# Optimization experiments

Hardware: AMD Instinct MI355X
Metric: run time of the kernel (lower is better)

The kernel has to match this reference:

```python
import jax, jax.numpy as jnp
import numpy as np

B, T, D, H, O = 4096, 512, 18, 8, 1


def setup_inputs() -> dict:
    key = jax.random.key(0)
    ks = jax.random.split(key, 8)
    x = jax.random.normal(ks[0], (B, T, D), dtype=jnp.float32)
    # PackedSequence invariant: lengths sorted descending, each >= 1
    lengths = jax.random.randint(ks[1], (B,), 1, T + 1, dtype=jnp.int32)
    lengths = jnp.sort(lengths)[::-1]
    s = 1.0 / np.sqrt(H)
    W_ih = jax.random.uniform(ks[2], (4 * H, D), jnp.float32, -s, s)
    W_hh = jax.random.uniform(ks[3], (4 * H, H), jnp.float32, -s, s)
    b_ih = jax.random.uniform(ks[4], (4 * H,), jnp.float32, -s, s)
    b_hh = jax.random.uniform(ks[5], (4 * H,), jnp.float32, -s, s)
    W_lin = jax.random.uniform(ks[6], (O, H), jnp.float32, -s, s)
    b_lin = jax.random.uniform(ks[7], (O,), jnp.float32, -s, s)
    return {"x": x, "lengths": lengths, "W_ih": W_ih, "W_hh": W_hh,
            "b_ih": b_ih, "b_hh": b_hh, "W_lin": W_lin, "b_lin": b_lin}


def reference(x, lengths, W_ih, W_hh, b_ih, b_hh, W_lin, b_lin):
    # Single-layer LSTM over ragged (packed) sequences, zero init hidden,
    # then a Linear head on every valid timestep (squash_packed).
    bias = b_ih + b_hh  # [4H]
    xg = jnp.einsum('btd,gd->btg', x, W_ih) + bias  # precompute input gates [B,T,4H]
    xg_t = jnp.swapaxes(xg, 0, 1)  # [T,B,4H]
    # mask[t,b] = t < lengths[b]  (packed steps actually computed)
    mask = (jnp.arange(T)[:, None] < lengths[None, :])[..., None]  # [T,B,1]

    h0 = jnp.zeros((B, H), x.dtype)
    c0 = jnp.zeros((B, H), x.dtype)

    def step(carry, inp):
        h, c = carry
        g_x, m = inp  # [B,4H], [B,1]
        gates = g_x + h @ W_hh.T
        i, f, g, o = jnp.split(gates, 4, axis=-1)  # torch gate order i,f,g,o
        i = jax.nn.sigmoid(i); f = jax.nn.sigmoid(f); o = jax.nn.sigmoid(o)
        g = jnp.tanh(g)
        c_new = f * c + i * g
        h_new = o * jnp.tanh(c_new)
        # beyond a sequence's length the packed LSTM never updates its state
        h = jnp.where(m, h_new, h)
        c = jnp.where(m, c_new, c)
        return (h, c), jnp.where(m, h_new, 0.0)

    (_, _), hs = jax.lax.scan(step, (h0, c0), (xg_t, mask))  # hs: [T,B,H]
    hs = jnp.swapaxes(hs, 0, 1)  # [B,T,H]
    y = jnp.einsum('bth,oh->bto', hs, W_lin) + b_lin  # [B,T,O]
    # linear head only applied to valid (packed) entries; zero out padding
    pad_mask = jnp.swapaxes(mask, 0, 1)  # [B,T,1]
    return jnp.where(pad_mask, y, 0.0)
```

## Files before the change

### kernel.cpp

```cpp
#include <hip/hip_runtime.h>


namespace {

constexpr int NT = 512;
constexpr int ND = 18;
constexpr float LOG2E = 1.4426950408889634f;

typedef float v2f __attribute__((ext_vector_type(2)));
typedef float v4f __attribute__((ext_vector_type(4)));

template <int C>
__device__ __forceinline__ float fdpp(float v) {
    const int i = __float_as_int(v);
    return __int_as_float(__builtin_amdgcn_update_dpp(i, i, C, 0xF, 0xF, true));
}
__device__ __forceinline__ void gload_lds(const void* g, void* l) {
    __builtin_amdgcn_global_load_lds(
        (const __attribute__((address_space(1))) void*)g,
        (__attribute__((address_space(3))) void*)l, 4, 0, 0);
}

__global__ __launch_bounds__(128, 1) void lstm_pc(
    const float* __restrict__ x, const int* __restrict__ lengths,
    const float* __restrict__ W_ih, const float* __restrict__ W_hh,
    const float* __restrict__ b_ih, const float* __restrict__ b_hh,
    const float* __restrict__ W_lin, const float* __restrict__ b_lin,
    float* __restrict__ out)
{
    __shared__ __align__(16) float Aring[32][4][16];
    __shared__ __align__(16) float Bring[4][8][4][2];
    __shared__ __align__(16) v2f   XG[4][8][16][5];

    const int tid  = (int)threadIdx.x;
    const int wav  = tid >> 6;
    const int w    = tid & 63;
    const int grp  = w >> 4;
    const int l16  = w & 15;
    const int p    = l16 >> 3;
    const int j    = l16 & 7;
    const int lenmax = lengths[blockIdx.x * 4];
    const int nwin = (lenmax + 15) >> 4;
    const int rowA = j + (p ? 8 : 0);
    const int rowB = j + (p ? 24 : 16);

    if (wav == 1) {
        v2f wxA[9], wxB[9];
        {
            const v2f* ra = (const v2f*)(W_ih + rowA * ND);
            const v2f* rb = (const v2f*)(W_ih + rowB * ND);
#pragma unroll
            for (int k = 0; k < 9; ++k) { wxA[k] = ra[k]; wxB[k] = rb[k]; }
        }
        const float biasA = b_ih[rowA] + b_hh[rowA];
        const float biasB = b_ih[rowB] + b_hh[rowB];

        const char* xc = (const char*)x;
        const char* pA = xc + (size_t)((((unsigned)(blockIdx.x * 4 + (w >> 4)) * (NT * ND))
                                       + (unsigned)(w & 15)) * 4u);
        const char* pB = xc + (size_t)((((unsigned)(blockIdx.x * 4 + ((w >> 1) & 3)) * (NT * ND))
                                       + 16u + (unsigned)(w & 1)) * 4u);
        const unsigned rB0 = (unsigned)(w >> 3);

        auto dma_chunk = [&](int dd) {
            const int r0 = dd * 8;
#pragma unroll
            for (int k = 0; k < 8; ++k) {
                const int rr = (r0 + k < NT) ? (r0 + k) : (NT - 1);
                gload_lds(pA + (unsigned)rr * 72u, &Aring[(r0 + k) & 31][0][0]);
            }
            unsigned rb = (unsigned)r0 + rB0;
            rb = (rb < (unsigned)NT) ? rb : (unsigned)(NT - 1);
            gload_lds(pB + rb * 72u, &Bring[dd & 3][0][0][0]);
        };

        auto produce_chunk = [&](int cc) {
            const int s0 = (cc * 8) & 31;
            const int bf = cc & 3;
#pragma unroll
            for (int k = 0; k < 8; ++k) {
                const v4f* ap = (const v4f*)&Aring[s0 + k][grp][0];
                const v4f q0 = ap[0], q1 = ap[1], q2 = ap[2], q3 = ap[3];
                const v2f bt = *(const v2f*)&Bring[bf][k][grp][0];
                v2f aA = v2f{biasA, 0.f}, aB = v2f{biasB, 0.f};
                aA = q0.lo * wxA[0] + aA;  aB = q0.lo * wxB[0] + aB;
                aA = q0.hi * wxA[1] + aA;  aB = q0.hi * wxB[1] + aB;
                aA = q1.lo * wxA[2] + aA;  aB = q1.lo * wxB[2] + aB;
                aA = q1.hi * wxA[3] + aA;  aB = q1.hi * wxB[3] + aB;
                aA = q2.lo * wxA[4] + aA;  aB = q2.lo * wxB[4] + aB;
                aA = q2.hi * wxA[5] + aA;  aB = q2.hi * wxB[5] + aB;
                aA = q3.lo * wxA[6] + aA;  aB = q3.lo * wxB[6] + aB;
                aA = q3.hi * wxA[7] + aA;  aB = q3.hi * wxB[7] + aB;
                aA = bt * wxA[8] + aA;     aB = bt * wxB[8] + aB;
                XG[bf][k][l16][grp] = v2f{aA.x + aA.y, aB.x + aB.y};
            }
        };

        dma_chunk(0); dma_chunk(1); dma_chunk(2); dma_chunk(3);
        asm volatile("s_waitcnt vmcnt(18)" ::: "memory");
        produce_chunk(0);
        produce_chunk(1);
        asm volatile("s_waitcnt lgkmcnt(0)" ::: "memory");
        __builtin_amdgcn_sched_barrier(0);
        __builtin_amdgcn_s_barrier();
        __builtin_amdgcn_sched_barrier(0);

        for (int I = 0; I < nwin; ++I) {
            dma_chunk(2 * I + 4);
            dma_chunk(2 * I + 5);
            asm volatile("s_waitcnt vmcnt(18)" ::: "memory");
            produce_chunk(2 * I + 2);
            produce_chunk(2 * I + 3);
            asm volatile("s_waitcnt lgkmcnt(0)" ::: "memory");
            __builtin_amdgcn_sched_barrier(0);
            __builtin_amdgcn_s_barrier();
            __builtin_amdgcn_sched_barrier(0);
        }
    } else {
        const int len = lengths[blockIdx.x * 4 + grp];

        int idx[8];
        idx[0] = j;
        idx[1] = __builtin_amdgcn_update_dpp(0, j, 0x121, 0xF, 0xF, true) & 7;
        idx[2] = __builtin_amdgcn_update_dpp(0, j, 0x122, 0xF, 0xF, true) & 7;
        idx[3] = __builtin_amdgcn_update_dpp(0, j, 0x123, 0xF, 0xF, true) & 7;
        idx[4] = __builtin_amdgcn_update_dpp(0, j, 0x124, 0xF, 0xF, true) & 7;
        idx[5] = __builtin_amdgcn_update_dpp(0, j, 0x125, 0xF, 0xF, true) & 7;
        idx[6] = __builtin_amdgcn_update_dpp(0, j, 0x126, 0xF, 0xF, true) & 7;
        idx[7] = __builtin_amdgcn_update_dpp(0, j, 0x127, 0xF, 0xF, true) & 7;

        v2f whA[4], whB[4], wl2[4];
#pragma unroll
        for (int r = 0; r < 4; ++r) {
            whA[r] = v2f{W_hh[rowA * 8 + idx[2 * r]], W_hh[rowA * 8 + idx[2 * r + 1]]};
            whB[r] = v2f{W_hh[rowB * 8 + idx[2 * r]], W_hh[rowB * 8 + idx[2 * r + 1]]};
            wl2[r] = v2f{W_lin[idx[2 * r]], W_lin[idx[2 * r + 1]]};
        }
        const float bl = b_lin[0];
        const float Kp = p ? -LOG2E : -2.0f * LOG2E;

        float* yb = out + (size_t)(blockIdx.x * 4 + grp) * NT;

        v2f hp[4] = {v2f{0.f, 0.f}, v2f{0.f, 0.f}, v2f{0.f, 0.f}, v2f{0.f, 0.f}};
        float c_ = 0.0f, hown = 0.0f;

        __builtin_amdgcn_s_barrier();
        __builtin_amdgcn_sched_barrier(0);

        for (int I = 0; I < nwin; ++I) {
            const int t = I * 16;
            const v2f* xg0 = &XG[(2 * I) & 3][0][l16][grp];
            const v2f* xg1 = &XG[(2 * I + 1) & 3][0][l16][grp];
            float y[16];
            v2f xgn = xg0[0];
#pragma unroll
            for (int k = 0; k < 16; ++k) {
                const v2f xgc = xgn;
                if (k < 15) xgn = (k + 1 < 8) ? xg0[(k + 1) * 80] : xg1[(k + 1 - 8) * 80];

                v2f tA = hp[0] * whA[0];
                tA = hp[1] * whA[1] + tA;
                tA = hp[2] * whA[2] + tA;
                tA = hp[3] * whA[3] + tA;
                v2f tB = hp[0] * whB[0];
                tB = hp[1] * whB[1] + tB;
                tB = hp[2] * whB[2] + tB;
                tB = hp[3] * whB[3] + tB;
                const float aA = (xgc.x + tA.x) + tA.y;
                const float aB = (xgc.y + tB.x) + tB.y;

                const float vA = __builtin_amdgcn_rcpf(
                    1.0f + __builtin_amdgcn_exp2f(aA * -LOG2E));
                const float sB = __builtin_amdgcn_rcpf(
                    1.0f + __builtin_amdgcn_exp2f(aB * Kp));
                const float vB = p ? sB : fmaf(2.0f, sB, -1.0f);

                const float send1 = p ? vA : (vA * vB);
                const float ex1 = fdpp<0x128>(send1);
                const float f_ = p ? send1 : ex1;
                const float ig_ = p ? ex1 : send1;
                c_ = fmaf(f_, c_, ig_);
                const float tc = fmaf(-2.0f, __builtin_amdgcn_rcpf(
                    1.0f + __builtin_amdgcn_exp2f(c_ * (2.0f * LOG2E))), 1.0f);
                const float ex2 = fdpp<0x128>(vB);
                const float o_ = p ? vB : ex2;
                hown = o_ * tc;

                const float h1 = fdpp<0x121>(hown);
                const float h2 = fdpp<0x122>(hown);
                const float h3 = fdpp<0x123>(hown);
                const float h4 = fdpp<0x124>(hown);
                const float h5 = fdpp<0x125>(hown);
                const float h6 = fdpp<0x126>(hown);
                const float h7 = fdpp<0x127>(hown);
                hp[0] = v2f{hown, h1}; hp[1] = v2f{h2, h3};
                hp[2] = v2f{h4, h5};   hp[3] = v2f{h6, h7};

                v2f ya = hp[0] * wl2[0];
                ya = hp[1] * wl2[1] + ya;
                ya = hp[2] * wl2[2] + ya;
                ya = hp[3] * wl2[3] + ya;
                y[k] = (ya.x + ya.y) + bl;
            }

            if (l16 == 0) {
                if (t + 15 < len) {
                    *(v4f*)(yb + t)      = v4f{y[0],  y[1],  y[2],  y[3]};
                    *(v4f*)(yb + t + 4)  = v4f{y[4],  y[5],  y[6],  y[7]};
                    *(v4f*)(yb + t + 8)  = v4f{y[8],  y[9],  y[10], y[11]};
                    *(v4f*)(yb + t + 12) = v4f{y[12], y[13], y[14], y[15]};
                } else {
#pragma unroll
                    for (int k = 0; k < 16; ++k)
                        if (t + k < len) yb[t + k] = y[k];
                }
            }
            __builtin_amdgcn_sched_barrier(0);
            __builtin_amdgcn_s_barrier();
            __builtin_amdgcn_sched_barrier(0);
        }
    }
}

}

extern "C" void kernel_launch(void* const* d_in, const int* in_sizes, int n_in,
                              void* d_out, int out_size, void* d_ws, size_t ws_size,
                              hipStream_t stream) {
    const float* x     = (const float*)d_in[0];
    const int*   lens  = (const int*)d_in[1];
    const float* W_ih  = (const float*)d_in[2];
    const float* W_hh  = (const float*)d_in[3];
    const float* b_ih  = (const float*)d_in[4];
    const float* b_hh  = (const float*)d_in[5];
    const float* W_lin = (const float*)d_in[6];
    const float* b_lin = (const float*)d_in[7];
    float* out = (float*)d_out;

    hipMemsetAsync(out, 0, (size_t)4096 * NT * sizeof(float), stream);

    lstm_pc<<<1024, 128, 0, stream>>>(x, lens, W_ih, W_hh, b_ih, b_hh,
                                      W_lin, b_lin, out);
}
```

Before: 78.87 us.

## Process eight sequences per block with one lane per hidden unit

Changes the work mapping so each block handles 8 sequences instead of 4, and each lane owns one hidden unit and computes all four gates itself. Before, a pair of lanes split the gates and exchanged them with DPP. The hidden state is broadcast with shuffles, and blocks are paired long/short through a reversed index to balance the sorted lengths. This halves the grid to 512 blocks and removes cross-lane gate exchanges. In return each lane does twice the recurrent FMAs and four transcendentals per step on the serial critical path, and shuffles replace the cheaper DPP row moves.

```diff
diff --git a/kernel.cpp b/kernel.cpp
--- a/kernel.cpp
+++ b/kernel.cpp
@@ -10,56 +10,53 @@
 typedef float v2f __attribute__((ext_vector_type(2)));
 typedef float v4f __attribute__((ext_vector_type(4)));
 
-template <int C>
-__device__ __forceinline__ float fdpp(float v) {
-    const int i = __float_as_int(v);
-    return __int_as_float(__builtin_amdgcn_update_dpp(i, i, C, 0xF, 0xF, true));
-}
 __device__ __forceinline__ void gload_lds(const void* g, void* l) {
     __builtin_amdgcn_global_load_lds(
         (const __attribute__((address_space(1))) void*)g,
         (__attribute__((address_space(3))) void*)l, 4, 0, 0);
 }
 
-__global__ __launch_bounds__(128, 1) void lstm_pc(
+__global__ __launch_bounds__(128, 1) void lstm_pc8(
     const float* __restrict__ x, const int* __restrict__ lengths,
     const float* __restrict__ W_ih, const float* __restrict__ W_hh,
     const float* __restrict__ b_ih, const float* __restrict__ b_hh,
     const float* __restrict__ W_lin, const float* __restrict__ b_lin,
     float* __restrict__ out)
 {
-    __shared__ __align__(16) float Aring[32][4][16];
-    __shared__ __align__(16) float Bring[4][8][4][2];
-    __shared__ __align__(16) v2f   XG[4][8][16][5];
-
-    const int tid  = (int)threadIdx.x;
-    const int wav  = tid >> 6;
-    const int w    = tid & 63;
-    const int grp  = w >> 4;
-    const int l16  = w & 15;
-    const int p    = l16 >> 3;
-    const int j    = l16 & 7;
-    const int lenmax = lengths[blockIdx.x * 4];
+    __shared__ __align__(16) float Aring[32][8][16];
+    __shared__ __align__(16) float Bring[4][2][8][4][2];
+    __shared__ __align__(16) v4f   XG[4][8][8][8];
+
+    const int q_ = (int)blockIdx.x & 255;
+    const int g  = ((int)blockIdx.x >> 8) ? (511 - q_) : q_;
+
+    const int tid = (int)threadIdx.x;
+    const int wav = tid >> 6;
+    const int w   = tid & 63;
+    const int s   = w >> 3;
+    const int j   = w & 7;
+    const int lenmax = lengths[g * 8];
     const int nwin = (lenmax + 15) >> 4;
-    const int rowA = j + (p ? 8 : 0);
-    const int rowB = j + (p ? 24 : 16);
 
     if (wav == 1) {
-        v2f wxA[9], wxB[9];
-        {
-            const v2f* ra = (const v2f*)(W_ih + rowA * ND);
-            const v2f* rb = (const v2f*)(W_ih + rowB * ND);
-#pragma unroll
-            for (int k = 0; k < 9; ++k) { wxA[k] = ra[k]; wxB[k] = rb[k]; }
-        }
-        const float biasA = b_ih[rowA] + b_hh[rowA];
-        const float biasB = b_ih[rowB] + b_hh[rowB];
+        v2f wxIF[ND], wxGO[ND];
+#pragma unroll
+        for (int k = 0; k < ND; ++k) {
+            wxIF[k] = v2f{W_ih[j * ND + k],        W_ih[(8 + j) * ND + k]};
+            wxGO[k] = v2f{W_ih[(16 + j) * ND + k], W_ih[(24 + j) * ND + k]};
+        }
+        const v2f bIF = v2f{b_ih[j] + b_hh[j],           b_ih[8 + j] + b_hh[8 + j]};
+        const v2f bGO = v2f{b_ih[16 + j] + b_hh[16 + j], b_ih[24 + j] + b_hh[24 + j]};
 
         const char* xc = (const char*)x;
-        const char* pA = xc + (size_t)((((unsigned)(blockIdx.x * 4 + (w >> 4)) * (NT * ND))
-                                       + (unsigned)(w & 15)) * 4u);
-        const char* pB = xc + (size_t)((((unsigned)(blockIdx.x * 4 + ((w >> 1) & 3)) * (NT * ND))
-                                       + 16u + (unsigned)(w & 1)) * 4u);
+        const char* pA1 = xc + (size_t)((((unsigned)(g * 8 + (w >> 4)) * (NT * ND))
+                                        + (unsigned)(w & 15)) * 4u);
+        const char* pA2 = xc + (size_t)((((unsigned)(g * 8 + 4 + (w >> 4)) * (NT * ND))
+                                        + (unsigned)(w & 15)) * 4u);
+        const char* pB1 = xc + (size_t)((((unsigned)(g * 8 + ((w >> 1) & 3)) * (NT * ND))
+                                        + 16u + (unsigned)(w & 1)) * 4u);
+        const char* pB2 = xc + (size_t)((((unsigned)(g * 8 + 4 + ((w >> 1) & 3)) * (NT * ND))
+                                        + 16u + (unsigned)(w & 1)) * 4u);
         const unsigned rB0 = (unsigned)(w >> 3);
 
         auto dma_chunk = [&](int dd) {
@@ -67,11 +64,13 @@
 #pragma unroll
             for (int k = 0; k < 8; ++k) {
                 const int rr = (r0 + k < NT) ? (r0 + k) : (NT - 1);
-                gload_lds(pA + (unsigned)rr * 72u, &Aring[(r0 + k) & 31][0][0]);
+                gload_lds(pA1 + (unsigned)rr * 72u, &Aring[(r0 + k) & 31][0][0]);
+                gload_lds(pA2 + (unsigned)rr * 72u, &Aring[(r0 + k) & 31][4][0]);
             }
             unsigned rb = (unsigned)r0 + rB0;
             rb = (rb < (unsigned)NT) ? rb : (unsigned)(NT - 1);
-            gload_lds(pB + rb * 72u, &Bring[dd & 3][0][0][0]);
+            gload_lds(pB1 + rb * 72u, &Bring[dd & 3][0][0][0][0]);
+            gload_lds(pB2 + rb * 72u, &Bring[dd & 3][1][0][0][0]);
         };
 
         auto produce_chunk = [&](int cc) {
@@ -79,25 +78,34 @@
             const int bf = cc & 3;
 #pragma unroll
             for (int k = 0; k < 8; ++k) {
-                const v4f* ap = (const v4f*)&Aring[s0 + k][grp][0];
+                const v4f* ap = (const v4f*)&Aring[s0 + k][s][0];
                 const v4f q0 = ap[0], q1 = ap[1], q2 = ap[2], q3 = ap[3];
-                const v2f bt = *(const v2f*)&Bring[bf][k][grp][0];
-                v2f aA = v2f{biasA, 0.f}, aB = v2f{biasB, 0.f};
-                aA = q0.lo * wxA[0] + aA;  aB = q0.lo * wxB[0] + aB;
-                aA = q0.hi * wxA[1] + aA;  aB = q0.hi * wxB[1] + aB;
-                aA = q1.lo * wxA[2] + aA;  aB = q1.lo * wxB[2] + aB;
-                aA = q1.hi * wxA[3] + aA;  aB = q1.hi * wxB[3] + aB;
-                aA = q2.lo * wxA[4] + aA;  aB = q2.lo * wxB[4] + aB;
-                aA = q2.hi * wxA[5] + aA;  aB = q2.hi * wxB[5] + aB;
-                aA = q3.lo * wxA[6] + aA;  aB = q3.lo * wxB[6] + aB;
-                aA = q3.hi * wxA[7] + aA;  aB = q3.hi * wxB[7] + aB;
-                aA = bt * wxA[8] + aA;     aB = bt * wxB[8] + aB;
-                XG[bf][k][l16][grp] = v2f{aA.x + aA.y, aB.x + aB.y};
+                const v2f bt = *(const v2f*)&Bring[bf][s >> 2][k][s & 3][0];
+                v2f aIF = bIF, aGO = bGO;
+                aIF = q0.x * wxIF[0]  + aIF;  aGO = q0.x * wxGO[0]  + aGO;
+                aIF = q0.y * wxIF[1]  + aIF;  aGO = q0.y * wxGO[1]  + aGO;
+                aIF = q0.z * wxIF[2]  + aIF;  aGO = q0.z * wxGO[2]  + aGO;
+                aIF = q0.w * wxIF[3]  + aIF;  aGO = q0.w * wxGO[3]  + aGO;
+                aIF = q1.x * wxIF[4]  + aIF;  aGO = q1.x * wxGO[4]  + aGO;
+                aIF = q1.y * wxIF[5]  + aIF;  aGO = q1.y * wxGO[5]  + aGO;
+                aIF = q1.z * wxIF[6]  + aIF;  aGO = q1.z * wxGO[6]  + aGO;
+                aIF = q1.w * wxIF[7]  + aIF;  aGO = q1.w * wxGO[7]  + aGO;
+                aIF = q2.x * wxIF[8]  + aIF;  aGO = q2.x * wxGO[8]  + aGO;
+                aIF = q2.y * wxIF[9]  + aIF;  aGO = q2.y * wxGO[9]  + aGO;
+                aIF = q2.z * wxIF[10] + aIF;  aGO = q2.z * wxGO[10] + aGO;
+                aIF = q2.w * wxIF[11] + aIF;  aGO = q2.w * wxGO[11] + aGO;
+                aIF = q3.x * wxIF[12] + aIF;  aGO = q3.x * wxGO[12] + aGO;
+                aIF = q3.y * wxIF[13] + aIF;  aGO = q3.y * wxGO[13] + aGO;
+                aIF = q3.z * wxIF[14] + aIF;  aGO = q3.z * wxGO[14] + aGO;
+                aIF = q3.w * wxIF[15] + aIF;  aGO = q3.w * wxGO[15] + aGO;
+                aIF = bt.x * wxIF[16] + aIF;  aGO = bt.x * wxGO[16] + aGO;
+                aIF = bt.y * wxIF[17] + aIF;  aGO = bt.y * wxGO[17] + aGO;
+                XG[bf][k][s][j] = v4f{aIF.x, aIF.y, aGO.x, aGO.y};
             }
         };
 
         dma_chunk(0); dma_chunk(1); dma_chunk(2); dma_chunk(3);
-        asm volatile("s_waitcnt vmcnt(18)" ::: "memory");
+        asm volatile("s_waitcnt vmcnt(36)" ::: "memory");
         produce_chunk(0);
         produce_chunk(1);
         asm volatile("s_waitcnt lgkmcnt(0)" ::: "memory");
@@ -108,7 +116,7 @@
         for (int I = 0; I < nwin; ++I) {
             dma_chunk(2 * I + 4);
             dma_chunk(2 * I + 5);
-            asm volatile("s_waitcnt vmcnt(18)" ::: "memory");
+            asm volatile("s_waitcnt vmcnt(36)" ::: "memory");
             produce_chunk(2 * I + 2);
             produce_chunk(2 * I + 3);
             asm volatile("s_waitcnt lgkmcnt(0)" ::: "memory");
@@ -117,93 +125,86 @@
             __builtin_amdgcn_sched_barrier(0);
         }
     } else {
-        const int len = lengths[blockIdx.x * 4 + grp];
-
-        int idx[8];
-        idx[0] = j;
-        idx[1] = __builtin_amdgcn_update_dpp(0, j, 0x121, 0xF, 0xF, true) & 7;
-        idx[2] = __builtin_amdgcn_update_dpp(0, j, 0x122, 0xF, 0xF, true) & 7;
-        idx[3] = __builtin_amdgcn_update_dpp(0, j, 0x123, 0xF, 0xF, true) & 7;
-        idx[4] = __builtin_amdgcn_update_dpp(0, j, 0x124, 0xF, 0xF, true) & 7;
-        idx[5] = __builtin_amdgcn_update_dpp(0, j, 0x125, 0xF, 0xF, true) & 7;
-        idx[6] = __builtin_amdgcn_update_dpp(0, j, 0x126, 0xF, 0xF, true) & 7;
-        idx[7] = __builtin_amdgcn_update_dpp(0, j, 0x127, 0xF, 0xF, true) & 7;
-
-        v2f whA[4], whB[4], wl2[4];
-#pragma unroll
-        for (int r = 0; r < 4; ++r) {
-            whA[r] = v2f{W_hh[rowA * 8 + idx[2 * r]], W_hh[rowA * 8 + idx[2 * r + 1]]};
-            whB[r] = v2f{W_hh[rowB * 8 + idx[2 * r]], W_hh[rowB * 8 + idx[2 * r + 1]]};
-            wl2[r] = v2f{W_lin[idx[2 * r]], W_lin[idx[2 * r + 1]]};
-        }
+        const int len = lengths[g * 8 + s];
+
+        v2f whIF[8], whGO[8];
+#pragma unroll
+        for (int r = 0; r < 8; ++r) {
+            whIF[r] = v2f{W_hh[j * 8 + r],        W_hh[(8 + j) * 8 + r]};
+            whGO[r] = v2f{W_hh[(16 + j) * 8 + r], W_hh[(24 + j) * 8 + r]};
+        }
+        float wl[8];
+#pragma unroll
+        for (int r = 0; r < 8; ++r) wl[r] = W_lin[r];
         const float bl = b_lin[0];
-        const float Kp = p ? -LOG2E : -2.0f * LOG2E;
-
-        float* yb = out + (size_t)(blockIdx.x * 4 + grp) * NT;
-
-        v2f hp[4] = {v2f{0.f, 0.f}, v2f{0.f, 0.f}, v2f{0.f, 0.f}, v2f{0.f, 0.f}};
+
+        float* yb = out + (size_t)(g * 8 + s) * NT;
+
+        float h_all[8];
+#pragma unroll
+        for (int r = 0; r < 8; ++r) h_all[r] = 0.0f;
         float c_ = 0.0f, hown = 0.0f;
+        const int lbase = w & 56;
 
         __builtin_amdgcn_s_barrier();
         __builtin_amdgcn_sched_barrier(0);
 
         for (int I = 0; I < nwin; ++I) {
             const int t = I * 16;
-            const v2f* xg0 = &XG[(2 * I) & 3][0][l16][grp];
-            const v2f* xg1 = &XG[(2 * I + 1) & 3][0][l16][grp];
+            const v4f* xg0 = &XG[(2 * I) & 3][0][s][j];
+            const v4f* xg1 = &XG[(2 * I + 1) & 3][0][s][j];
             float y[16];
-            v2f xgn = xg0[0];
+            v4f xgn = xg0[0];
 #pragma unroll
             for (int k = 0; k < 16; ++k) {
-                const v2f xgc = xgn;
-                if (k < 15) xgn = (k + 1 < 8) ? xg0[(k + 1) * 80] : xg1[(k + 1 - 8) * 80];
-
-                v2f tA = hp[0] * whA[0];
-                tA = hp[1] * whA[1] + tA;
-                tA = hp[2] * whA[2] + tA;
-                tA = hp[3] * whA[3] + tA;
-                v2f tB = hp[0] * whB[0];
-                tB = hp[1] * whB[1] + tB;
-                tB = hp[2] * whB[2] + tB;
-                tB = hp[3] * whB[3] + tB;
-                const float aA = (xgc.x + tA.x) + tA.y;
-                const float aB = (xgc.y + tB.x) + tB.y;
-
-                const float vA = __builtin_amdgcn_rcpf(
-                    1.0f + __builtin_amdgcn_exp2f(aA * -LOG2E));
-                const float sB = __builtin_amdgcn_rcpf(
-                    1.0f + __builtin_amdgcn_exp2f(aB * Kp));
-                const float vB = p ? sB : fmaf(2.0f, sB, -1.0f);
-
-                const float send1 = p ? vA : (vA * vB);
-                const float ex1 = fdpp<0x128>(send1);
-                const float f_ = p ? send1 : ex1;
-                const float ig_ = p ? ex1 : send1;
-                c_ = fmaf(f_, c_, ig_);
+                const v4f xgc = xgn;
+                if (k < 15) xgn = (k + 1 < 8) ? xg0[(k + 1) * 64] : xg1[(k + 1 - 8) * 64];
+
+                v2f aIF = v2f{xgc.x, xgc.y}, aGO = v2f{xgc.z, xgc.w};
+                aIF = h_all[0] * whIF[0] + aIF;  aGO = h_all[0] * whGO[0] + aGO;
+                aIF = h_all[1] * whIF[1] + aIF;  aGO = h_all[1] * whGO[1] + aGO;
+                aIF = h_all[2] * whIF[2] + aIF;  aGO = h_all[2] * whGO[2] + aGO;
+                aIF = h_all[3] * whIF[3] + aIF;  aGO = h_all[3] * whGO[3] + aGO;
+                aIF = h_all[4] * whIF[4] + aIF;  aGO = h_all[4] * whGO[4] + aGO;
+                aIF = h_all[5] * whIF[5] + aIF;  aGO = h_all[5] * whGO[5] + aGO;
+                aIF = h_all[6] * whIF[6] + aIF;  aGO = h_all[6] * whGO[6] + aGO;
+                aIF = h_all[7] * whIF[7] + aIF;  aGO = h_all[7] * whGO[7] + aGO;
+
+                const float si = __builtin_amdgcn_rcpf(
+                    1.0f + __builtin_amdgcn_exp2f(aIF.x * -LOG2E));
+                const float sf = __builtin_amdgcn_rcpf(
+                    1.0f + __builtin_amdgcn_exp2f(aIF.y * -LOG2E));
+                const float tg = fmaf(2.0f, __builtin_amdgcn_rcpf(
+                    1.0f + __builtin_amdgcn_exp2f(aGO.x * (-2.0f * LOG2E))), -1.0f);
+                const float so = __builtin_amdgcn_rcpf(
+                    1.0f + __builtin_amdgcn_exp2f(aGO.y * -LOG2E));
+                c_ = fmaf(sf, c_, si * tg);
                 const float tc = fmaf(-2.0f, __builtin_amdgcn_rcpf(
                     1.0f + __builtin_amdgcn_exp2f(c_ * (2.0f * LOG2E))), 1.0f);
-                const float ex2 = fdpp<0x128>(vB);
-                const float o_ = p ? vB : ex2;
-                hown = o_ * tc;
-
-                const float h1 = fdpp<0x121>(hown);
-                const float h2 = fdpp<0x122>(hown);
-                const float h3 = fdpp<0x123>(hown);
-                const float h4 = fdpp<0x124>(hown);
-                const float h5 = fdpp<0x125>(hown);
-                const float h6 = fdpp<0x126>(hown);
-                const float h7 = fdpp<0x127>(hown);
-                hp[0] = v2f{hown, h1}; hp[1] = v2f{h2, h3};
-                hp[2] = v2f{h4, h5};   hp[3] = v2f{h6, h7};
-
-                v2f ya = hp[0] * wl2[0];
-                ya = hp[1] * wl2[1] + ya;
-                ya = hp[2] * wl2[2] + ya;
-                ya = hp[3] * wl2[3] + ya;
-                y[k] = (ya.x + ya.y) + bl;
-            }
-
-            if (l16 == 0) {
+                hown = so * tc;
+
+                h_all[0] = __shfl(hown, lbase | 0, 64);
+                h_all[1] = __shfl(hown, lbase | 1, 64);
+                h_all[2] = __shfl(hown, lbase | 2, 64);
+                h_all[3] = __shfl(hown, lbase | 3, 64);
+                h_all[4] = __shfl(hown, lbase | 4, 64);
+                h_all[5] = __shfl(hown, lbase | 5, 64);
+                h_all[6] = __shfl(hown, lbase | 6, 64);
+                h_all[7] = __shfl(hown, lbase | 7, 64);
+
+                float yv = bl;
+                yv = fmaf(h_all[0], wl[0], yv);
+                yv = fmaf(h_all[1], wl[1], yv);
+                yv = fmaf(h_all[2], wl[2], yv);
+                yv = fmaf(h_all[3], wl[3], yv);
+                yv = fmaf(h_all[4], wl[4], yv);
+                yv = fmaf(h_all[5], wl[5], yv);
+                yv = fmaf(h_all[6], wl[6], yv);
+                yv = fmaf(h_all[7], wl[7], yv);
+                y[k] = yv;
+            }
+
+            if (j == 0) {
                 if (t + 15 < len) {
                     *(v4f*)(yb + t)      = v4f{y[0],  y[1],  y[2],  y[3]};
                     *(v4f*)(yb + t + 4)  = v4f{y[4],  y[5],  y[6],  y[7]};
@@ -239,6 +240,6 @@
 
     hipMemsetAsync(out, 0, (size_t)4096 * NT * sizeof(float), stream);
 
-    lstm_pc<<<1024, 128, 0, stream>>>(x, lens, W_ih, W_hh, b_ih, b_hh,
+    lstm_pc8<<<512, 128, 0, stream>>>(x, lens, W_ih, W_hh, b_ih, b_hh,
                                       W_lin, b_lin, out);
 }
```

Result: slower. 105.5 us (+33.7%).
